# Performance work log

Hardware: AMD Instinct MI355X
Metric: run time of the kernel (lower is better)

## Reference

```python
import math
import jax, jax.numpy as jnp
import numpy as np

PRED_LEN = 96
K = 32
LOW_FREQ = 1


def setup_inputs() -> dict:
    key = jax.random.key(0)
    x = jax.random.normal(key, (8, 512, 512), dtype=jnp.float32)
    return {"x": x}


def _fourier_forward(x):
    b, t, d = x.shape
    # rFFT over time axis (always fp32, matching torch autocast-disabled block)
    x_freq = jnp.fft.rfft(x.astype(jnp.float32), axis=1)  # (b, t//2+1, d) complex64
    freqs = jnp.fft.rfftfreq(t).astype(jnp.float32)
    if t % 2 == 0:
        x_freq = x_freq[:, LOW_FREQ:-1]
        f = freqs[LOW_FREQ:-1]
    else:
        x_freq = x_freq[:, LOW_FREQ:]
        f = freqs[LOW_FREQ:]
    n_freq = x_freq.shape[1]
    k = min(K, n_freq)

    # top-k |X(f)| independently per (batch, channel): move freq to last axis
    mag = jnp.transpose(jnp.abs(x_freq), (0, 2, 1))          # (b, d, f)
    _, idx = jax.lax.top_k(mag, k)                            # (b, d, k)
    x_freq_t = jnp.transpose(x_freq, (0, 2, 1))               # (b, d, f)
    x_sel = jnp.transpose(jnp.take_along_axis(x_freq_t, idx, axis=2), (0, 2, 1))  # (b, k, d)
    f_sel = jnp.transpose(f[idx], (0, 2, 1))[:, :, None, :]   # (b, k, 1, d)

    # extrapolate: add conjugate (negative) frequencies
    x_full = jnp.concatenate([x_sel, jnp.conj(x_sel)], axis=1)  # (b, 2k, d)
    f_full = jnp.concatenate([f_sel, -f_sel], axis=1)           # (b, 2k, 1, d)
    t_val = jnp.arange(t + PRED_LEN, dtype=jnp.float32)[None, None, :, None]  # (1,1,T,1)
    amp = (jnp.abs(x_full) / t)[:, :, None, :]                  # (b, 2k, 1, d)
    phase = jnp.angle(x_full)[:, :, None, :]                    # (b, 2k, 1, d)
    x_time = amp * jnp.cos(2.0 * math.pi * f_full * t_val + phase)  # (b, 2k, T, d)
    return jnp.sum(x_time, axis=1)                              # (b, t+pred_len, d)


def reference(x):
    return _fourier_forward(x)
```

## Files before the change

kernel.cpp:

```cpp
#include <hip/hip_runtime.h>
#include <math.h>

#define BATCH 8
#define TLEN  512
#define DDIM  512
#define TOUT  608
#define KSEL  32
#define DT    8

#define TWO_PI_OVER_512 0.0122718463030851562f
#define SC (2.0f / 512.0f)

typedef __attribute__((ext_vector_type(8))) short short8;
typedef __attribute__((ext_vector_type(4))) float f32x4;

#define BMT_OFF 0
#define WK_OFF  4194304

__device__ __forceinline__ unsigned short f2bf(float f) {
    unsigned u = __float_as_uint(f);
    return (unsigned short)((u + 0x7FFF + ((u >> 16) & 1)) >> 16);
}

__device__ __constant__ const float CC16[16] = {
     1.f,  0.92387953251128674f,  0.70710678118654752f,  0.38268343236508977f,
     0.f, -0.38268343236508977f, -0.70710678118654752f, -0.92387953251128674f,
    -1.f, -0.92387953251128674f, -0.70710678118654752f, -0.38268343236508977f,
     0.f,  0.38268343236508977f,  0.70710678118654752f,  0.92387953251128674f };
__device__ __constant__ const float SS16[16] = {
     0.f,  0.38268343236508977f,  0.70710678118654752f,  0.92387953251128674f,
     1.f,  0.92387953251128674f,  0.70710678118654752f,  0.38268343236508977f,
     0.f, -0.38268343236508977f, -0.70710678118654752f, -0.92387953251128674f,
    -1.f, -0.92387953251128674f, -0.70710678118654752f, -0.38268343236508977f };

__global__ __launch_bounds__(512, 4) void fft_topk_kernel(const float* __restrict__ x,
                                                          unsigned short* __restrict__ BmT,
                                                          unsigned short* __restrict__ Wk,
                                                          float* __restrict__ out) {
    __shared__ __align__(16) unsigned char smem[42328];
    float2* Xl  = (float2*)smem;
    float*  xs  = (float*)smem;
    float*  ysr = (float*)(smem + 16448);
    float*  ysi = (float*)(smem + 27140);
    float2* tw  = (float2*)(smem + 37832);

    const int tid = threadIdx.x;
    const int bid = blockIdx.x;
    const int b   = bid >> 6;
    const int d0  = ((bid & 7) * 8 + ((bid >> 3) & 7)) * DT;

    {
        float s, c;
        sincosf((float)tid * TWO_PI_OVER_512, &s, &c);
        tw[tid] = make_float2(c, s);
    }

    {
        const float* xr = x + ((size_t)b * TLEN + tid) * DDIM + d0;
        float4 lo = *(const float4*)(xr);
        float4 hi = *(const float4*)(xr + 4);
        *(float4*)&xs[tid * 8]     = lo;
        *(float4*)&xs[tid * 8 + 4] = hi;
    }
    __syncthreads();

    {
        const int h   = tid >> 8;
        const int rem = tid & 255;
        const int aA  = rem >> 3;
        const int dA  = rem & 7;
        float xv[16];
        #pragma unroll
        for (int c = 0; c < 16; ++c)
            xv[c] = xs[(aA + 32 * c) * 8 + dA];

        if (h == 0) {
            #pragma unroll
            for (int q = 0; q <= 4; ++q) {
                float sr = 0.f, si = 0.f;
                #pragma unroll
                for (int c = 0; c < 16; ++c) {
                    const int n = (c * q) & 15;
                    sr = fmaf(xv[c],  CC16[n], sr);
                    si = fmaf(xv[c], -SS16[n], si);
                }
                ysr[(q * 33 + aA) * 9 + dA] = sr;
                ysi[(q * 33 + aA) * 9 + dA] = si;
            }
        } else {
            #pragma unroll
            for (int q = 5; q <= 8; ++q) {
                float sr = 0.f, si = 0.f;
                #pragma unroll
                for (int c = 0; c < 16; ++c) {
                    const int n = (c * q) & 15;
                    sr = fmaf(xv[c],  CC16[n], sr);
                    si = fmaf(xv[c], -SS16[n], si);
                }
                ysr[(q * 33 + aA) * 9 + dA] = sr;
                ysi[(q * 33 + aA) * 9 + dA] = si;
            }
        }
    }
    __syncthreads();

    {
        const int ahalf = tid & 1;
        const int dB    = (tid >> 1) & 7;
        const int kk    = tid >> 4;
        const int qp    = kk & 15;
        const int qrow  = (qp <= 8) ? qp : 16 - qp;
        const bool neg  = (qp > 8);

        const int ybase = (qrow * 33 + ahalf * 16) * 9 + dB;
        float Yr_[16], Yi_[16], Pr_[16], Pi_[16];
        #pragma unroll
        for (int aa = 0; aa < 16; ++aa) {
            Yr_[aa] = ysr[ybase + aa * 9];
            float yi = ysi[ybase + aa * 9];
            Yi_[aa] = neg ? -yi : yi;
        }
        #pragma unroll
        for (int aa = 0; aa < 16; ++aa) {
            const int arow = ahalf * 16 + aa;
            float2 w = tw[(arow * kk) & 511];
            Pr_[aa] = w.x;
            Pi_[aa] = -w.y;
        }

        float ar[8] = {}, ai[8] = {};
        #pragma unroll
        for (int aa = 0; aa < 16; ++aa) {
            float zr = Yr_[aa] * Pr_[aa] - Yi_[aa] * Pi_[aa];
            float zi = Yr_[aa] * Pi_[aa] + Yi_[aa] * Pr_[aa];
            #pragma unroll
            for (int u = 0; u < 8; ++u) {
                const int n = (aa * u) & 15;
                ar[u] = fmaf(zr, CC16[n], fmaf(zi,  SS16[n], ar[u]));
                ai[u] = fmaf(zi, CC16[n], fmaf(-zr, SS16[n], ai[u]));
            }
        }

        #pragma unroll
        for (int u = 0; u < 8; ++u) {
            ar[u] += __shfl_xor(ar[u], 1);
            ai[u] += __shfl_xor(ai[u], 1);
        }
        #pragma unroll
        for (int v = 0; v < 4; ++v) {
            const int u = ahalf * 4 + v;
            Xl[dB * 257 + kk + 32 * u] = make_float2(ar[u], ai[u]);
        }
    }
    __syncthreads();

    if (bid < 256 && tid < 256) {
        const int half = tid >> 7;
        const int j    = tid & 127;
        float2 w0 = tw[(bid * (2 * j)) & 511];
        float2 w1 = tw[(bid * (2 * j + 1)) & 511];
        unsigned val = half
            ? ((unsigned)f2bf(w0.y * SC) | ((unsigned)f2bf(w1.y * SC) << 16))
            : ((unsigned)f2bf(w0.x * SC) | ((unsigned)f2bf(w1.x * SC) << 16));
        *(unsigned*)&Wk[((size_t)bid << 9) + (half << 8) + 2 * j] = val;
    }

    {
        const int l  = tid & 63;
        const int dd = tid >> 6;
        const unsigned long long below = ((unsigned long long)1 << l) - 1;

        float zr[4], zi[4];
        unsigned vb[4];
        int mm[4];
        #pragma unroll
        for (int s = 0; s < 4; ++s) {
            int m = 1 + l + 64 * s;
            mm[s] = m;
            if (m <= 255) {
                float2 z = Xl[dd * 257 + m];
                zr[s] = z.x; zi[s] = z.y;
                vb[s] = __float_as_uint(fmaf(z.x, z.x, z.y * z.y));
            } else { zr[s] = 0.f; zi[s] = 0.f; vb[s] = 0u; }
        }

        unsigned tau = 0;
        #pragma unroll
        for (int bit = 29; bit >= 1; bit -= 2) {
            const unsigned c1 = tau | (1u << bit);
            const unsigned c2 = tau | (2u << bit);
            const unsigned c3 = tau | (3u << bit);
            int n1 = __popcll(__ballot(vb[0] >= c1)) + __popcll(__ballot(vb[1] >= c1))
                   + __popcll(__ballot(vb[2] >= c1)) + __popcll(__ballot(vb[3] >= c1));
            int n2 = __popcll(__ballot(vb[0] >= c2)) + __popcll(__ballot(vb[1] >= c2))
                   + __popcll(__ballot(vb[2] >= c2)) + __popcll(__ballot(vb[3] >= c2));
            int n3 = __popcll(__ballot(vb[0] >= c3)) + __popcll(__ballot(vb[1] >= c3))
                   + __popcll(__ballot(vb[2] >= c3)) + __popcll(__ballot(vb[3] >= c3));
            tau = (n3 >= KSEL) ? c3 : (n2 >= KSEL) ? c2 : (n1 >= KSEL) ? c1 : tau;
        }
        {
            const unsigned c = tau | 1u;
            int n = __popcll(__ballot(vb[0] >= c)) + __popcll(__ballot(vb[1] >= c))
                  + __popcll(__ballot(vb[2] >= c)) + __popcll(__ballot(vb[3] >= c));
            if (n >= KSEL) tau = c;
        }

        unsigned long long beq[4];
        int cgt = 0;
        #pragma unroll
        for (int s = 0; s < 4; ++s) {
            beq[s] = __ballot(vb[s] == tau);
            cgt += __popcll(__ballot(vb[s] > tau));
        }
        const int need = KSEL - cgt;

        unsigned short* Brow = BmT + ((size_t)(b * DDIM + d0 + dd) << 9);
        int be = 0;
        float dot = 0.f;
        #pragma unroll
        for (int s = 0; s < 4; ++s) {
            bool keep = (vb[s] > tau);
            if (vb[s] == tau) {
                int r = be + __popcll(beq[s] & below);
                keep = (r < need);
            }
            be += __popcll(beq[s]);
            const int mi = mm[s] & 255;
            Brow[mi]       = keep ? f2bf(zr[s]) : (unsigned short)0;
            Brow[256 + mi] = keep ? f2bf(zi[s]) : (unsigned short)0;
            if (keep) dot = fmaf(zr[s], (mm[s] & 1) ? -SC : SC, dot);
        }

        #pragma unroll
        for (int off = 1; off < 64; off <<= 1)
            dot += __shfl_xor(dot, off);
        if (l == 0)
            out[((size_t)b * TOUT + 256) * DDIM + d0 + dd] = dot;
    }
}

__global__ __launch_bounds__(512, 4) void gemm_kernel(const unsigned short* __restrict__ Wk,
                                                      const unsigned short* __restrict__ BmT,
                                                      float* __restrict__ out) {
    __shared__ unsigned short Al[64][136];
    __shared__ unsigned short Bl[64][136];

    const int tid = threadIdx.x;
    const int bid = blockIdx.x;
    const int bt  = bid >> 6;
    const int b   = (bid >> 3) & 7;
    const int bd  = bid & 7;

    const int wid  = tid >> 6;
    const int l    = tid & 63;
    const int wm   = wid & 3;
    const int wn   = wid >> 2;
    const int lrow = l & 15;
    const int lk8  = (l >> 4) * 8;

    const int srow = tid >> 3;
    const int soff = (tid & 7) * 8;

    const unsigned short* Wrow = Wk  + (size_t)(bt * 64 + srow) * 512 + soff;
    const unsigned short* Brow = BmT + ((size_t)(b * DDIM + bd * 64 + srow)) * 512 + soff;

    f32x4 accp0 = {0.f, 0.f, 0.f, 0.f};
    f32x4 accp1 = {0.f, 0.f, 0.f, 0.f};
    f32x4 accm0 = {0.f, 0.f, 0.f, 0.f};
    f32x4 accm1 = {0.f, 0.f, 0.f, 0.f};

    uint4 av0 = *(const uint4*)(Wrow);
    uint4 av1 = *(const uint4*)(Wrow + 64);
    uint4 bv0 = *(const uint4*)(Brow);
    uint4 bv1 = *(const uint4*)(Brow + 64);

    for (int kc = 0; kc < 512; kc += 128) {
        __syncthreads();
        *(uint4*)&Al[srow][soff]      = av0;
        *(uint4*)&Al[srow][soff + 64] = av1;
        *(uint4*)&Bl[srow][soff]      = bv0;
        *(uint4*)&Bl[srow][soff + 64] = bv1;
        __syncthreads();

        if (kc + 128 < 512) {
            av0 = *(const uint4*)(Wrow + kc + 128);
            av1 = *(const uint4*)(Wrow + kc + 192);
            bv0 = *(const uint4*)(Brow + kc + 128);
            bv1 = *(const uint4*)(Brow + kc + 192);
        }

        #pragma unroll
        for (int ks = 0; ks < 4; ++ks) {
            short8 af  = *(const short8*)&Al[wm * 16 + lrow][ks * 32 + lk8];
            short8 bf0 = *(const short8*)&Bl[wn * 32 + lrow][ks * 32 + lk8];
            short8 bf1 = *(const short8*)&Bl[wn * 32 + 16 + lrow][ks * 32 + lk8];
            const bool is_sin = (kc + ks * 32) >= 256;
            short8 afm = af;
            if (is_sin) afm ^= (short8)(short)0x8000;
            accp0 = __builtin_amdgcn_mfma_f32_16x16x32_bf16(af,  bf0, accp0, 0, 0, 0);
            accp1 = __builtin_amdgcn_mfma_f32_16x16x32_bf16(af,  bf1, accp1, 0, 0, 0);
            accm0 = __builtin_amdgcn_mfma_f32_16x16x32_bf16(afm, bf0, accm0, 0, 0, 0);
            accm1 = __builtin_amdgcn_mfma_f32_16x16x32_bf16(afm, bf1, accm1, 0, 0, 0);
        }
    }

    const int tg = bt * 64 + wm * 16 + (l >> 4) * 4;
    const int dg = bd * 64 + wn * 32 + (l & 15);
    float* ob = out + (size_t)b * TOUT * DDIM;
    #pragma unroll
    for (int r = 0; r < 4; ++r) {
        const int t  = tg + r;
        const int rp = 512 - t;
        ob[(size_t)t * DDIM + dg]       = accm0[r];
        ob[(size_t)t * DDIM + dg + 16]  = accm1[r];
        ob[(size_t)rp * DDIM + dg]      = accp0[r];
        ob[(size_t)rp * DDIM + dg + 16] = accp1[r];
        if (t < 96) {
            ob[(size_t)(t + 512) * DDIM + dg]      = accm0[r];
            ob[(size_t)(t + 512) * DDIM + dg + 16] = accm1[r];
        }
    }
}

extern "C" void kernel_launch(void* const* d_in, const int* in_sizes, int n_in,
                              void* d_out, int out_size, void* d_ws, size_t ws_size,
                              hipStream_t stream) {
    const float* x   = (const float*)d_in[0];
    float*       out = (float*)d_out;
    unsigned short* BmT = (unsigned short*)((char*)d_ws + BMT_OFF);
    unsigned short* Wk  = (unsigned short*)((char*)d_ws + WK_OFF);

    fft_topk_kernel<<<BATCH * 64, 512, 0, stream>>>(x, BmT, Wk, out);
    gemm_kernel<<<256, 512, 0, stream>>>(Wk, BmT, out);
}
```

Measured before the change: 22.97 us.

## Fuse FFT/top-k and GEMM into one kernel with inter-block flag sync

```diff
diff --git a/kernel.cpp b/kernel.cpp
--- a/kernel.cpp
+++ b/kernel.cpp
@@ -10,12 +10,13 @@
 
 #define TWO_PI_OVER_512 0.0122718463030851562f
 #define SC (2.0f / 512.0f)
+#define MAGIC 0x5F3C0D1Eu
 
 typedef __attribute__((ext_vector_type(8))) short short8;
 typedef __attribute__((ext_vector_type(4))) float f32x4;
 
-#define BMT_OFF 0
-#define WK_OFF  4194304
+#define BMT_OFF  0
+#define FLAG_OFF 4194304
 
 __device__ __forceinline__ unsigned short f2bf(float f) {
     unsigned u = __float_as_uint(f);
@@ -33,291 +34,315 @@
      0.f, -0.38268343236508977f, -0.70710678118654752f, -0.92387953251128674f,
     -1.f, -0.92387953251128674f, -0.70710678118654752f, -0.38268343236508977f };
 
-__global__ __launch_bounds__(512, 4) void fft_topk_kernel(const float* __restrict__ x,
-                                                          unsigned short* __restrict__ BmT,
-                                                          unsigned short* __restrict__ Wk,
-                                                          float* __restrict__ out) {
+__global__ __launch_bounds__(512, 4) void fourier_fused(const float* __restrict__ x,
+                                                        unsigned short* __restrict__ BmT,
+                                                        unsigned* __restrict__ flags,
+                                                        float* __restrict__ out) {
     __shared__ __align__(16) unsigned char smem[42328];
     float2* Xl  = (float2*)smem;
     float*  xs  = (float*)smem;
     float*  ysr = (float*)(smem + 16448);
     float*  ysi = (float*)(smem + 27140);
     float2* tw  = (float2*)(smem + 37832);
+    unsigned short* Al = (unsigned short*)smem;
+    unsigned short* Bl = (unsigned short*)(smem + 17408);
 
     const int tid = threadIdx.x;
     const int bid = blockIdx.x;
-    const int b   = bid >> 6;
-    const int d0  = ((bid & 7) * 8 + ((bid >> 3) & 7)) * DT;
 
     {
-        float s, c;
-        sincosf((float)tid * TWO_PI_OVER_512, &s, &c);
-        tw[tid] = make_float2(c, s);
-    }
-
-    {
-        const float* xr = x + ((size_t)b * TLEN + tid) * DDIM + d0;
-        float4 lo = *(const float4*)(xr);
-        float4 hi = *(const float4*)(xr + 4);
-        *(float4*)&xs[tid * 8]     = lo;
-        *(float4*)&xs[tid * 8 + 4] = hi;
+        const int b  = bid >> 6;
+        const int d0 = ((bid & 7) * 8 + ((bid >> 3) & 7)) * DT;
+
+        {
+            float s, c;
+            sincosf((float)tid * TWO_PI_OVER_512, &s, &c);
+            tw[tid] = make_float2(c, s);
+        }
+
+        {
+            const float* xr = x + ((size_t)b * TLEN + tid) * DDIM + d0;
+            float4 lo = *(const float4*)(xr);
+            float4 hi = *(const float4*)(xr + 4);
+            *(float4*)&xs[tid * 8]     = lo;
+            *(float4*)&xs[tid * 8 + 4] = hi;
+        }
+        __syncthreads();
+
+        {
+            const int h   = tid >> 8;
+            const int rem = tid & 255;
+            const int aA  = rem >> 3;
+            const int dA  = rem & 7;
+            float xv[16];
+            #pragma unroll
+            for (int c = 0; c < 16; ++c)
+                xv[c] = xs[(aA + 32 * c) * 8 + dA];
+
+            if (h == 0) {
+                #pragma unroll
+                for (int q = 0; q <= 4; ++q) {
+                    float sr = 0.f, si = 0.f;
+                    #pragma unroll
+                    for (int c = 0; c < 16; ++c) {
+                        const int n = (c * q) & 15;
+                        sr = fmaf(xv[c],  CC16[n], sr);
+                        si = fmaf(xv[c], -SS16[n], si);
+                    }
+                    ysr[(q * 33 + aA) * 9 + dA] = sr;
+                    ysi[(q * 33 + aA) * 9 + dA] = si;
+                }
+            } else {
+                #pragma unroll
+                for (int q = 5; q <= 8; ++q) {
+                    float sr = 0.f, si = 0.f;
+                    #pragma unroll
+                    for (int c = 0; c < 16; ++c) {
+                        const int n = (c * q) & 15;
+                        sr = fmaf(xv[c],  CC16[n], sr);
+                        si = fmaf(xv[c], -SS16[n], si);
+                    }
+                    ysr[(q * 33 + aA) * 9 + dA] = sr;
+                    ysi[(q * 33 + aA) * 9 + dA] = si;
+                }
+            }
+        }
+        __syncthreads();
+
+        {
+            const int ahalf = tid & 1;
+            const int dB    = (tid >> 1) & 7;
+            const int kk    = tid >> 4;
+            const int qp    = kk & 15;
+            const int qrow  = (qp <= 8) ? qp : 16 - qp;
+            const bool neg  = (qp > 8);
+
+            const int ybase = (qrow * 33 + ahalf * 16) * 9 + dB;
+            float Yr_[16], Yi_[16], Pr_[16], Pi_[16];
+            #pragma unroll
+            for (int aa = 0; aa < 16; ++aa) {
+                Yr_[aa] = ysr[ybase + aa * 9];
+                float yi = ysi[ybase + aa * 9];
+                Yi_[aa] = neg ? -yi : yi;
+            }
+            #pragma unroll
+            for (int aa = 0; aa < 16; ++aa) {
+                const int arow = ahalf * 16 + aa;
+                float2 w = tw[(arow * kk) & 511];
+                Pr_[aa] = w.x;
+                Pi_[aa] = -w.y;
+            }
+
+            float ar[8] = {}, ai[8] = {};
+            #pragma unroll
+            for (int aa = 0; aa < 16; ++aa) {
+                float zr = Yr_[aa] * Pr_[aa] - Yi_[aa] * Pi_[aa];
+                float zi = Yr_[aa] * Pi_[aa] + Yi_[aa] * Pr_[aa];
+                #pragma unroll
+                for (int u = 0; u < 8; ++u) {
+                    const int n = (aa * u) & 15;
+                    ar[u] = fmaf(zr, CC16[n], fmaf(zi,  SS16[n], ar[u]));
+                    ai[u] = fmaf(zi, CC16[n], fmaf(-zr, SS16[n], ai[u]));
+                }
+            }
+
+            #pragma unroll
+            for (int u = 0; u < 8; ++u) {
+                ar[u] += __shfl_xor(ar[u], 1);
+                ai[u] += __shfl_xor(ai[u], 1);
+            }
+            #pragma unroll
+            for (int v = 0; v < 4; ++v) {
+                const int u = ahalf * 4 + v;
+                Xl[dB * 257 + kk + 32 * u] = make_float2(ar[u], ai[u]);
+            }
+        }
+        __syncthreads();
+
+        {
+            const int l  = tid & 63;
+            const int dd = tid >> 6;
+            const unsigned long long below = ((unsigned long long)1 << l) - 1;
+
+            float zr[4], zi[4];
+            unsigned vb[4];
+            int mm[4];
+            #pragma unroll
+            for (int s = 0; s < 4; ++s) {
+                int m = 1 + l + 64 * s;
+                mm[s] = m;
+                if (m <= 255) {
+                    float2 z = Xl[dd * 257 + m];
+                    zr[s] = z.x; zi[s] = z.y;
+                    vb[s] = __float_as_uint(fmaf(z.x, z.x, z.y * z.y));
+                } else { zr[s] = 0.f; zi[s] = 0.f; vb[s] = 0u; }
+            }
+
+            unsigned tau = 0;
+            #pragma unroll
+            for (int bit = 29; bit >= 1; bit -= 2) {
+                const unsigned c1 = tau | (1u << bit);
+                const unsigned c2 = tau | (2u << bit);
+                const unsigned c3 = tau | (3u << bit);
+                int n1 = __popcll(__ballot(vb[0] >= c1)) + __popcll(__ballot(vb[1] >= c1))
+                       + __popcll(__ballot(vb[2] >= c1)) + __popcll(__ballot(vb[3] >= c1));
+                int n2 = __popcll(__ballot(vb[0] >= c2)) + __popcll(__ballot(vb[1] >= c2))
+                       + __popcll(__ballot(vb[2] >= c2)) + __popcll(__ballot(vb[3] >= c2));
+                int n3 = __popcll(__ballot(vb[0] >= c3)) + __popcll(__ballot(vb[1] >= c3))
+                       + __popcll(__ballot(vb[2] >= c3)) + __popcll(__ballot(vb[3] >= c3));
+                tau = (n3 >= KSEL) ? c3 : (n2 >= KSEL) ? c2 : (n1 >= KSEL) ? c1 : tau;
+            }
+            {
+                const unsigned c = tau | 1u;
+                int n = __popcll(__ballot(vb[0] >= c)) + __popcll(__ballot(vb[1] >= c))
+                      + __popcll(__ballot(vb[2] >= c)) + __popcll(__ballot(vb[3] >= c));
+                if (n >= KSEL) tau = c;
+            }
+
+            unsigned long long beq[4];
+            int cgt = 0;
+            #pragma unroll
+            for (int s = 0; s < 4; ++s) {
+                beq[s] = __ballot(vb[s] == tau);
+                cgt += __popcll(__ballot(vb[s] > tau));
+            }
+            const int need = KSEL - cgt;
+
+            unsigned short* Brow = BmT + ((size_t)(b * DDIM + d0 + dd) << 9);
+            int be = 0;
+            float dot = 0.f;
+            #pragma unroll
+            for (int s = 0; s < 4; ++s) {
+                bool keep = (vb[s] > tau);
+                if (vb[s] == tau) {
+                    int r = be + __popcll(beq[s] & below);
+                    keep = (r < need);
+                }
+                be += __popcll(beq[s]);
+                const int mi = mm[s] & 255;
+                Brow[mi]       = keep ? f2bf(zr[s]) : (unsigned short)0;
+                Brow[256 + mi] = keep ? f2bf(zi[s]) : (unsigned short)0;
+                if (keep) dot = fmaf(zr[s], (mm[s] & 1) ? -SC : SC, dot);
+            }
+
+            #pragma unroll
+            for (int off = 1; off < 64; off <<= 1)
+                dot += __shfl_xor(dot, off);
+            if (l == 0)
+                out[((size_t)b * TOUT + 256) * DDIM + d0 + dd] = dot;
+        }
     }
     __syncthreads();
 
+    if (tid == 0)
+        __hip_atomic_store(&flags[bid], MAGIC, __ATOMIC_RELEASE,
+                           __HIP_MEMORY_SCOPE_AGENT);
+
+    if (bid >= 256) return;
+
     {
-        const int h   = tid >> 8;
-        const int rem = tid & 255;
-        const int aA  = rem >> 3;
-        const int dA  = rem & 7;
-        float xv[16];
+        const int bt = bid >> 6;
+        const int b2 = (bid >> 3) & 7;
+        const int bd = bid & 7;
+
+        if (tid < 8) {
+            unsigned* f = flags + (b2 * 64 + bd);
+            while (__hip_atomic_load(&f[tid * 8], __ATOMIC_ACQUIRE,
+                                     __HIP_MEMORY_SCOPE_AGENT) != MAGIC)
+                __builtin_amdgcn_s_sleep(2);
+        }
+        __syncthreads();
+
+        const int wid  = tid >> 6;
+        const int l    = tid & 63;
+        const int wm   = wid & 3;
+        const int wn   = wid >> 2;
+        const int lrow = l & 15;
+        const int lk8  = (l >> 4) * 8;
+
+        const int srow = tid >> 3;
+        const int soff = (tid & 7) * 8;
+        const int trow = bt * 64 + srow;
+
+        const unsigned short* Brow =
+            BmT + ((size_t)(b2 * DDIM + bd * 64 + srow)) * 512 + soff;
+
+        f32x4 accp0 = {0.f, 0.f, 0.f, 0.f};
+        f32x4 accp1 = {0.f, 0.f, 0.f, 0.f};
+        f32x4 accm0 = {0.f, 0.f, 0.f, 0.f};
+        f32x4 accm1 = {0.f, 0.f, 0.f, 0.f};
+
+        uint4 bv0 = *(const uint4*)(Brow);
+        uint4 bv1 = *(const uint4*)(Brow + 64);
+
         #pragma unroll
-        for (int c = 0; c < 16; ++c)
-            xv[c] = xs[(aA + 32 * c) * 8 + dA];
-
-        if (h == 0) {
-            #pragma unroll
-            for (int q = 0; q <= 4; ++q) {
-                float sr = 0.f, si = 0.f;
+        for (int kci = 0; kci < 4; ++kci) {
+            const int kc = kci * 128;
+            const bool kind_sin = (kc >= 256);
+
+            uint4 av0, av1;
+            {
+                unsigned* a0 = (unsigned*)&av0;
+                unsigned* a1 = (unsigned*)&av1;
                 #pragma unroll
-                for (int c = 0; c < 16; ++c) {
-                    const int n = (c * q) & 15;
-                    sr = fmaf(xv[c],  CC16[n], sr);
-                    si = fmaf(xv[c], -SS16[n], si);
-                }
-                ysr[(q * 33 + aA) * 9 + dA] = sr;
-                ysi[(q * 33 + aA) * 9 + dA] = si;
-            }
-        } else {
-            #pragma unroll
-            for (int q = 5; q <= 8; ++q) {
-                float sr = 0.f, si = 0.f;
-                #pragma unroll
-                for (int c = 0; c < 16; ++c) {
-                    const int n = (c * q) & 15;
-                    sr = fmaf(xv[c],  CC16[n], sr);
-                    si = fmaf(xv[c], -SS16[n], si);
-                }
-                ysr[(q * 33 + aA) * 9 + dA] = sr;
-                ysi[(q * 33 + aA) * 9 + dA] = si;
-            }
-        }
-    }
-    __syncthreads();
-
-    {
-        const int ahalf = tid & 1;
-        const int dB    = (tid >> 1) & 7;
-        const int kk    = tid >> 4;
-        const int qp    = kk & 15;
-        const int qrow  = (qp <= 8) ? qp : 16 - qp;
-        const bool neg  = (qp > 8);
-
-        const int ybase = (qrow * 33 + ahalf * 16) * 9 + dB;
-        float Yr_[16], Yi_[16], Pr_[16], Pi_[16];
+                for (int d = 0; d < 4; ++d) {
+                    unsigned short v[4];
+                    #pragma unroll
+                    for (int e = 0; e < 2; ++e) {
+                        int col0 = kc + soff + 2 * d + e;
+                        int col1 = kc + 64 + soff + 2 * d + e;
+                        float s0, c0, s1, c1;
+                        sincosf((float)((trow * (col0 & 255)) & 511) * TWO_PI_OVER_512, &s0, &c0);
+                        sincosf((float)((trow * (col1 & 255)) & 511) * TWO_PI_OVER_512, &s1, &c1);
+                        v[e]     = f2bf((kind_sin ? s0 : c0) * SC);
+                        v[2 + e] = f2bf((kind_sin ? s1 : c1) * SC);
+                    }
+                    a0[d] = (unsigned)v[0] | ((unsigned)v[1] << 16);
+                    a1[d] = (unsigned)v[2] | ((unsigned)v[3] << 16);
+                }
+            }
+
+            __syncthreads();
+            *(uint4*)&Al[srow * 136 + soff]      = av0;
+            *(uint4*)&Al[srow * 136 + soff + 64] = av1;
+            *(uint4*)&Bl[srow * 136 + soff]      = bv0;
+            *(uint4*)&Bl[srow * 136 + soff + 64] = bv1;
+            __syncthreads();
+
+            if (kci < 3) {
+                bv0 = *(const uint4*)(Brow + kc + 128);
+                bv1 = *(const uint4*)(Brow + kc + 192);
+            }
+
+            #pragma unroll
+            for (int ks = 0; ks < 4; ++ks) {
+                short8 af  = *(const short8*)&Al[(wm * 16 + lrow) * 136 + ks * 32 + lk8];
+                short8 bf0 = *(const short8*)&Bl[(wn * 32 + lrow) * 136 + ks * 32 + lk8];
+                short8 bf1 = *(const short8*)&Bl[(wn * 32 + 16 + lrow) * 136 + ks * 32 + lk8];
+                short8 afm = af;
+                if (kind_sin) afm ^= (short8)(short)0x8000;
+                accp0 = __builtin_amdgcn_mfma_f32_16x16x32_bf16(af,  bf0, accp0, 0, 0, 0);
+                accp1 = __builtin_amdgcn_mfma_f32_16x16x32_bf16(af,  bf1, accp1, 0, 0, 0);
+                accm0 = __builtin_amdgcn_mfma_f32_16x16x32_bf16(afm, bf0, accm0, 0, 0, 0);
+                accm1 = __builtin_amdgcn_mfma_f32_16x16x32_bf16(afm, bf1, accm1, 0, 0, 0);
+            }
+        }
+
+        const int tg = bt * 64 + wm * 16 + (l >> 4) * 4;
+        const int dg = bd * 64 + wn * 32 + (l & 15);
+        float* ob = out + (size_t)b2 * TOUT * DDIM;
         #pragma unroll
-        for (int aa = 0; aa < 16; ++aa) {
-            Yr_[aa] = ysr[ybase + aa * 9];
-            float yi = ysi[ybase + aa * 9];
-            Yi_[aa] = neg ? -yi : yi;
-        }
-        #pragma unroll
-        for (int aa = 0; aa < 16; ++aa) {
-            const int arow = ahalf * 16 + aa;
-            float2 w = tw[(arow * kk) & 511];
-            Pr_[aa] = w.x;
-            Pi_[aa] = -w.y;
-        }
-
-        float ar[8] = {}, ai[8] = {};
-        #pragma unroll
-        for (int aa = 0; aa < 16; ++aa) {
-            float zr = Yr_[aa] * Pr_[aa] - Yi_[aa] * Pi_[aa];
-            float zi = Yr_[aa] * Pi_[aa] + Yi_[aa] * Pr_[aa];
-            #pragma unroll
-            for (int u = 0; u < 8; ++u) {
-                const int n = (aa * u) & 15;
-                ar[u] = fmaf(zr, CC16[n], fmaf(zi,  SS16[n], ar[u]));
-                ai[u] = fmaf(zi, CC16[n], fmaf(-zr, SS16[n], ai[u]));
-            }
-        }
-
-        #pragma unroll
-        for (int u = 0; u < 8; ++u) {
-            ar[u] += __shfl_xor(ar[u], 1);
-            ai[u] += __shfl_xor(ai[u], 1);
-        }
-        #pragma unroll
-        for (int v = 0; v < 4; ++v) {
-            const int u = ahalf * 4 + v;
-            Xl[dB * 257 + kk + 32 * u] = make_float2(ar[u], ai[u]);
-        }
-    }
-    __syncthreads();
-
-    if (bid < 256 && tid < 256) {
-        const int half = tid >> 7;
-        const int j    = tid & 127;
-        float2 w0 = tw[(bid * (2 * j)) & 511];
-        float2 w1 = tw[(bid * (2 * j + 1)) & 511];
-        unsigned val = half
-            ? ((unsigned)f2bf(w0.y * SC) | ((unsigned)f2bf(w1.y * SC) << 16))
-            : ((unsigned)f2bf(w0.x * SC) | ((unsigned)f2bf(w1.x * SC) << 16));
-        *(unsigned*)&Wk[((size_t)bid << 9) + (half << 8) + 2 * j] = val;
-    }
-
-    {
-        const int l  = tid & 63;
-        const int dd = tid >> 6;
-        const unsigned long long below = ((unsigned long long)1 << l) - 1;
-
-        float zr[4], zi[4];
-        unsigned vb[4];
-        int mm[4];
-        #pragma unroll
-        for (int s = 0; s < 4; ++s) {
-            int m = 1 + l + 64 * s;
-            mm[s] = m;
-            if (m <= 255) {
-                float2 z = Xl[dd * 257 + m];
-                zr[s] = z.x; zi[s] = z.y;
-                vb[s] = __float_as_uint(fmaf(z.x, z.x, z.y * z.y));
-            } else { zr[s] = 0.f; zi[s] = 0.f; vb[s] = 0u; }
-        }
-
-        unsigned tau = 0;
-        #pragma unroll
-        for (int bit = 29; bit >= 1; bit -= 2) {
-            const unsigned c1 = tau | (1u << bit);
-            const unsigned c2 = tau | (2u << bit);
-            const unsigned c3 = tau | (3u << bit);
-            int n1 = __popcll(__ballot(vb[0] >= c1)) + __popcll(__ballot(vb[1] >= c1))
-                   + __popcll(__ballot(vb[2] >= c1)) + __popcll(__ballot(vb[3] >= c1));
-            int n2 = __popcll(__ballot(vb[0] >= c2)) + __popcll(__ballot(vb[1] >= c2))
-                   + __popcll(__ballot(vb[2] >= c2)) + __popcll(__ballot(vb[3] >= c2));
-            int n3 = __popcll(__ballot(vb[0] >= c3)) + __popcll(__ballot(vb[1] >= c3))
-                   + __popcll(__ballot(vb[2] >= c3)) + __popcll(__ballot(vb[3] >= c3));
-            tau = (n3 >= KSEL) ? c3 : (n2 >= KSEL) ? c2 : (n1 >= KSEL) ? c1 : tau;
-        }
-        {
-            const unsigned c = tau | 1u;
-            int n = __popcll(__ballot(vb[0] >= c)) + __popcll(__ballot(vb[1] >= c))
-                  + __popcll(__ballot(vb[2] >= c)) + __popcll(__ballot(vb[3] >= c));
-            if (n >= KSEL) tau = c;
-        }
-
-        unsigned long long beq[4];
-        int cgt = 0;
-        #pragma unroll
-        for (int s = 0; s < 4; ++s) {
-            beq[s] = __ballot(vb[s] == tau);
-            cgt += __popcll(__ballot(vb[s] > tau));
-        }
-        const int need = KSEL - cgt;
-
-        unsigned short* Brow = BmT + ((size_t)(b * DDIM + d0 + dd) << 9);
-        int be = 0;
-        float dot = 0.f;
-        #pragma unroll
-        for (int s = 0; s < 4; ++s) {
-            bool keep = (vb[s] > tau);
-            if (vb[s] == tau) {
-                int r = be + __popcll(beq[s] & below);
-                keep = (r < need);
-            }
-            be += __popcll(beq[s]);
-            const int mi = mm[s] & 255;
-            Brow[mi]       = keep ? f2bf(zr[s]) : (unsigned short)0;
-            Brow[256 + mi] = keep ? f2bf(zi[s]) : (unsigned short)0;
-            if (keep) dot = fmaf(zr[s], (mm[s] & 1) ? -SC : SC, dot);
-        }
-
-        #pragma unroll
-        for (int off = 1; off < 64; off <<= 1)
-            dot += __shfl_xor(dot, off);
-        if (l == 0)
-            out[((size_t)b * TOUT + 256) * DDIM + d0 + dd] = dot;
-    }
-}
-
-__global__ __launch_bounds__(512, 4) void gemm_kernel(const unsigned short* __restrict__ Wk,
-                                                      const unsigned short* __restrict__ BmT,
-                                                      float* __restrict__ out) {
-    __shared__ unsigned short Al[64][136];
-    __shared__ unsigned short Bl[64][136];
-
-    const int tid = threadIdx.x;
-    const int bid = blockIdx.x;
-    const int bt  = bid >> 6;
-    const int b   = (bid >> 3) & 7;
-    const int bd  = bid & 7;
-
-    const int wid  = tid >> 6;
-    const int l    = tid & 63;
-    const int wm   = wid & 3;
-    const int wn   = wid >> 2;
-    const int lrow = l & 15;
-    const int lk8  = (l >> 4) * 8;
-
-    const int srow = tid >> 3;
-    const int soff = (tid & 7) * 8;
-
-    const unsigned short* Wrow = Wk  + (size_t)(bt * 64 + srow) * 512 + soff;
-    const unsigned short* Brow = BmT + ((size_t)(b * DDIM + bd * 64 + srow)) * 512 + soff;
-
-    f32x4 accp0 = {0.f, 0.f, 0.f, 0.f};
-    f32x4 accp1 = {0.f, 0.f, 0.f, 0.f};
-    f32x4 accm0 = {0.f, 0.f, 0.f, 0.f};
-    f32x4 accm1 = {0.f, 0.f, 0.f, 0.f};
-
-    uint4 av0 = *(const uint4*)(Wrow);
-    uint4 av1 = *(const uint4*)(Wrow + 64);
-    uint4 bv0 = *(const uint4*)(Brow);
-    uint4 bv1 = *(const uint4*)(Brow + 64);
-
-    for (int kc = 0; kc < 512; kc += 128) {
-        __syncthreads();
-        *(uint4*)&Al[srow][soff]      = av0;
-        *(uint4*)&Al[srow][soff + 64] = av1;
-        *(uint4*)&Bl[srow][soff]      = bv0;
-        *(uint4*)&Bl[srow][soff + 64] = bv1;
-        __syncthreads();
-
-        if (kc + 128 < 512) {
-            av0 = *(const uint4*)(Wrow + kc + 128);
-            av1 = *(const uint4*)(Wrow + kc + 192);
-            bv0 = *(const uint4*)(Brow + kc + 128);
-            bv1 = *(const uint4*)(Brow + kc + 192);
-        }
-
-        #pragma unroll
-        for (int ks = 0; ks < 4; ++ks) {
-            short8 af  = *(const short8*)&Al[wm * 16 + lrow][ks * 32 + lk8];
-            short8 bf0 = *(const short8*)&Bl[wn * 32 + lrow][ks * 32 + lk8];
-            short8 bf1 = *(const short8*)&Bl[wn * 32 + 16 + lrow][ks * 32 + lk8];
-            const bool is_sin = (kc + ks * 32) >= 256;
-            short8 afm = af;
-            if (is_sin) afm ^= (short8)(short)0x8000;
-            accp0 = __builtin_amdgcn_mfma_f32_16x16x32_bf16(af,  bf0, accp0, 0, 0, 0);
-            accp1 = __builtin_amdgcn_mfma_f32_16x16x32_bf16(af,  bf1, accp1, 0, 0, 0);
-            accm0 = __builtin_amdgcn_mfma_f32_16x16x32_bf16(afm, bf0, accm0, 0, 0, 0);
-            accm1 = __builtin_amdgcn_mfma_f32_16x16x32_bf16(afm, bf1, accm1, 0, 0, 0);
-        }
-    }
-
-    const int tg = bt * 64 + wm * 16 + (l >> 4) * 4;
-    const int dg = bd * 64 + wn * 32 + (l & 15);
-    float* ob = out + (size_t)b * TOUT * DDIM;
-    #pragma unroll
-    for (int r = 0; r < 4; ++r) {
-        const int t  = tg + r;
-        const int rp = 512 - t;
-        ob[(size_t)t * DDIM + dg]       = accm0[r];
-        ob[(size_t)t * DDIM + dg + 16]  = accm1[r];
-        ob[(size_t)rp * DDIM + dg]      = accp0[r];
-        ob[(size_t)rp * DDIM + dg + 16] = accp1[r];
-        if (t < 96) {
-            ob[(size_t)(t + 512) * DDIM + dg]      = accm0[r];
-            ob[(size_t)(t + 512) * DDIM + dg + 16] = accm1[r];
+        for (int r = 0; r < 4; ++r) {
+            const int t  = tg + r;
+            const int rp = 512 - t;
+            ob[(size_t)t * DDIM + dg]       = accm0[r];
+            ob[(size_t)t * DDIM + dg + 16]  = accm1[r];
+            ob[(size_t)rp * DDIM + dg]      = accp0[r];
+            ob[(size_t)rp * DDIM + dg + 16] = accp1[r];
+            if (t < 96) {
+                ob[(size_t)(t + 512) * DDIM + dg]      = accm0[r];
+                ob[(size_t)(t + 512) * DDIM + dg + 16] = accm1[r];
+            }
         }
     }
 }
@@ -327,9 +352,8 @@
                               hipStream_t stream) {
     const float* x   = (const float*)d_in[0];
     float*       out = (float*)d_out;
-    unsigned short* BmT = (unsigned short*)((char*)d_ws + BMT_OFF);
-    unsigned short* Wk  = (unsigned short*)((char*)d_ws + WK_OFF);
-
-    fft_topk_kernel<<<BATCH * 64, 512, 0, stream>>>(x, BmT, Wk, out);
-    gemm_kernel<<<256, 512, 0, stream>>>(Wk, BmT, out);
+    unsigned short* BmT   = (unsigned short*)((char*)d_ws + BMT_OFF);
+    unsigned*       flags = (unsigned*)((char*)d_ws + FLAG_OFF);
+
+    fourier_fused<<<512, 512, 0, stream>>>(x, BmT, flags, out);
 }
```

Result: slower. 37.65 us (+63.9%).
